# Performance work log

Measured on AMD Instinct MI355X. Metric: run time of the kernel, lower is better.

The kernel has to match this reference:

```python
import jax, jax.numpy as jnp
import numpy as np

NSUB = 2          # fixed RK4 substeps per output interval (deterministic stand-in for adaptive dopri5)
SLOPE = 1.0 / 5.5  # leaky_relu negative slope used by g and OutputNN


def setup_inputs() -> dict:
    key = jax.random.key(0)
    ks = iter(jax.random.split(key, 40))
    B, Tp, Tf = 256, 32, 256
    D, H, HF, HG, HO = 1, 100, 275, 75, 75

    def rn(shape, s=0.05):
        return jax.random.normal(next(ks), shape, jnp.float32) * s

    # past: [B, Tp, 1+D] with strictly increasing times in column 0
    past_t = jnp.sort(jax.random.uniform(next(ks), (B, Tp), jnp.float32) * Tp, axis=1)
    past_x = jax.random.normal(next(ks), (B, Tp, D), jnp.float32)
    past = jnp.concatenate([past_t[:, :, None], past_x], axis=2)
    # future times start after the last past time, strictly increasing
    t_future = past_t[:, -1:] + jnp.sort(
        jax.random.uniform(next(ks), (B, Tf), jnp.float32) * 0.1 * Tf, axis=1)

    return dict(
        past=past,
        h0=jnp.zeros((B, H), jnp.float32),
        t_future=t_future,
        eps=jax.random.normal(next(ks), (H, B), jnp.float32),
        fW1=rn((HF, H + 1)), fb1=rn((HF,)), fW2=rn((HF, HF)), fb2=rn((HF,)),
        fW3=rn((H, HF)), fb3=rn((H,)),
        gru_Wih=rn((3 * H, D)), gru_Whh=rn((3 * H, H)),
        gru_bih=rn((3 * H,)), gru_bhh=rn((3 * H,)),
        gW1=rn((HG, H)), gb1=rn((HG,)), gW2=rn((HG, HG)), gb2=rn((HG,)),
        gW3=rn((2, HG)), gb3=rn((2,)),
        oW1=rn((HO, H)), ob1=rn((HO,)), oW2=rn((HO, HO)), ob2=rn((HO,)),
        oW3=rn((D, HO)), ob3=rn((D,)),
    )


def _leaky(x):
    return jnp.where(x >= 0, x, SLOPE * x)


def reference(past, h0, t_future, eps,
              fW1, fb1, fW2, fb2, fW3, fb3,
              gru_Wih, gru_Whh, gru_bih, gru_bhh,
              gW1, gb1, gW2, gb2, gW3, gb3,
              oW1, ob1, oW2, ob2, oW3, ob3):
    def field(t, y):  # t: [B], y: [B, H] -> dy/dt: [B, H]  (f module)
        x = jnp.concatenate([t[:, None], y], axis=1)
        x = jnp.tanh(x @ fW1.T + fb1)
        x = jnp.tanh(x @ fW2.T + fb2)
        return jnp.tanh(x @ fW3.T + fb3)

    def integrate(y0, t0, t1):  # batched fixed-step RK4 from t0 to t1 (per-batch times)
        dt = ((t1 - t0) / NSUB)[:, None]  # [B, 1]
        dts = dt[:, 0]
        def body(y, i):
            t = t0 + i * dts
            k1 = field(t, y)
            k2 = field(t + 0.5 * dts, y + 0.5 * dt * k1)
            k3 = field(t + 0.5 * dts, y + 0.5 * dt * k2)
            k4 = field(t + dts, y + dt * k3)
            return y + dt * (k1 + 2.0 * k2 + 2.0 * k3 + k4) / 6.0, None
        y, _ = jax.lax.scan(body, y0, jnp.arange(NSUB, dtype=y0.dtype))
        return y

    def gru(x, h):  # torch.nn.GRUCell math
        gi = x @ gru_Wih.T + gru_bih
        gh = h @ gru_Whh.T + gru_bhh
        ir, iz, inn = jnp.split(gi, 3, axis=1)
        hr, hz, hn = jnp.split(gh, 3, axis=1)
        r = jax.nn.sigmoid(ir + hr)
        z = jax.nn.sigmoid(iz + hz)
        n = jnp.tanh(inn + r * hn)
        return (1.0 - z) * n + z * h

    times = past[:, :, 0]   # [B, Tp]
    data = past[:, :, 1:]   # [B, Tp, D]

    # first GRUODE step: evolve h0 from t0-1 to t0, then GRU update with x0
    h = gru(data[:, 0], integrate(h0, times[:, 0] - 1.0, times[:, 0]))
    xs = (jnp.swapaxes(data[:, 1:], 0, 1), times[:, :-1].T, times[:, 1:].T)
    def pbody(hc, s):
        x, tp, tc = s
        return gru(x, integrate(hc, tp, tc)), None
    h, _ = jax.lax.scan(pbody, h, xs)

    # g head -> (loc, |scale|), reproducing the concat/view of the original
    gx = _leaky(h @ gW1.T + gb1)
    gx = _leaky(gx @ gW2.T + gb2)
    gx = gx @ gW3.T + gb3                                   # [B, 2]
    pr = jnp.concatenate([gx[:, 0], jnp.abs(gx[:, 1])]).reshape(-1, 2)
    loc, scale = pr[:, 0], pr[:, 1]                          # [B], [B]

    # Sampler: Normal(loc, scale).rsample([H]) reparameterized with eps [H, B]
    z0 = (loc[None, :] + scale[None, :] * eps).T             # [B, H]

    # integrate z0 across future time grid
    def fbody(y, s):
        tp, tc = s
        yn = integrate(y, tp, tc)
        return yn, yn
    _, traj = jax.lax.scan(fbody, z0, (t_future[:, :-1].T, t_future[:, 1:].T))
    out = jnp.swapaxes(jnp.concatenate([z0[None], traj], axis=0), 0, 1)  # [B, Tf, H]

    # OutputNN head
    o = _leaky(out @ oW1.T + ob1)
    o = _leaky(o @ oW2.T + ob2)
    return o @ oW3.T + ob3  # [B, Tf, D]
```

## Files before the change

### kernel.cpp

```cpp
#include <hip/hip_runtime.h>
#include <hip/hip_fp16.h>

typedef _Float16 f16;
typedef _Float16 f16x2 __attribute__((ext_vector_type(2)));
typedef _Float16 f16x8 __attribute__((ext_vector_type(8)));
typedef float f32x4 __attribute__((ext_vector_type(4)));
typedef unsigned short u16;
typedef unsigned int u32;

__device__ __forceinline__ float fdot2v(f16x2 a, f16x2 b, float c){
#if __has_builtin(__builtin_amdgcn_fdot2)
  return __builtin_amdgcn_fdot2(a, b, c, false);
#else
  return c + (float)a.x * (float)b.x + (float)a.y * (float)b.y;
#endif
}

__device__ __forceinline__ float rcp_f(float x){
#if __has_builtin(__builtin_amdgcn_rcpf)
  return __builtin_amdgcn_rcpf(x);
#else
  return 1.f / x;
#endif
}

__device__ __forceinline__ float tanh_f(float x){
  return 1.f - 2.f * rcp_f(__expf(2.f * x) + 1.f);
}
__device__ __forceinline__ float sigm_f(float x){
  return rcp_f(1.f + __expf(-x));
}
__device__ __forceinline__ float leaky_f(float x){
  return x >= 0.f ? x : x * (1.0f / 5.5f);
}

template<int NP>
__device__ __forceinline__ void ld_pairs(const float* W, int row, int ncols, int c0,
                                         f16x2* dst, bool valid){
  const float* base = W + (long)row * ncols;
#pragma unroll
  for (int p = 0; p < NP; p++){
    int c = c0 + 2 * p;
    f16x2 v;
    v.x = (valid && c     < ncols) ? (f16)base[c]     : (f16)0.f;
    v.y = (valid && c + 1 < ncols) ? (f16)base[c + 1] : (f16)0.f;
    dst[p] = v;
  }
}

template<int NCH>
__device__ __forceinline__ float dot_chunks(const f16x2* w, const f16x8* x, int chunk0){
  float a0 = 0.f, a1 = 0.f, a2 = 0.f, a3 = 0.f;
#pragma unroll
  for (int c = 0; c < NCH; c++){
    union { f16x8 v; f16x2 h[4]; } u;
    u.v = x[chunk0 + c];
    a0 = fdot2v(w[4*c + 0], u.h[0], a0);
    a1 = fdot2v(w[4*c + 1], u.h[1], a1);
    a2 = fdot2v(w[4*c + 2], u.h[2], a2);
    a3 = fdot2v(w[4*c + 3], u.h[3], a3);
  }
  return (a0 + a1) + (a2 + a3);
}

__device__ __forceinline__ f16x8 ldfrag(const float* W, int row, int ncols, int k0, bool valid){
  f16x8 v;
#pragma unroll
  for (int j = 0; j < 8; j++){
    int c = k0 + j;
    v[j] = (valid && c < ncols) ? (f16)W[(long)row * ncols + c] : (f16)0.f;
  }
  return v;
}

__device__ __forceinline__ float sel4(f32x4 a, int c){
  float v = a.x;
  v = (c == 1) ? a.y : v;
  v = (c == 2) ? a.z : v;
  v = (c == 3) ? a.w : v;
  return v;
}
__device__ __forceinline__ float selacc(f32x4 a0, f32x4 a1, int lm){
  f32x4 t;
  t.x = (lm & 4) ? a1.x : a0.x;
  t.y = (lm & 4) ? a1.y : a0.y;
  t.z = (lm & 4) ? a1.z : a0.z;
  t.w = (lm & 4) ? a1.w : a0.w;
  return sel4(t, lm & 3);
}

#define MFMA16(A,B,C) __builtin_amdgcn_mfma_f32_16x16x32_f16((A),(B),(C),0,0,0)

struct FRM {
  f16x8 a1[2][4];
  f16x8 a2[2][9];
  f16x8 a3[9];
  f16x2 w1b[4];
  f16x2 w2b[9];
  float w1tb, b1bv, b2bv;
  float w1tw, b1w, b2w;
  float b3w;
};

struct DEC {
  f16x2 dW1[16]; f16x2 dW2[12]; f16x2 dW3;
  float ob1v, ob2v, ob3v;
};

__device__ __forceinline__ void load_field_mfma(FRM& R, int tid,
    const float* fW1, const float* fb1, const float* fW2, const float* fb2,
    const float* fW3, const float* fb3)
{
  const int lane = tid & 63, wv = tid >> 6;
  const int lm = lane & 15, lg = lane >> 4;
  const int r0 = 32 * wv + lm, r1 = r0 + 16;
#pragma unroll
  for (int c = 0; c < 4; c++){
    R.a1[0][c] = ldfrag(fW1, r0, 101, 32 * c + 8 * lg, true);
    R.a1[1][c] = ldfrag(fW1, r1, 101, 32 * c + 8 * lg, true);
  }
#pragma unroll
  for (int c = 0; c < 9; c++){
    R.a2[0][c] = ldfrag(fW2, r0, 275, 32 * c + 8 * lg, true);
    R.a2[1][c] = ldfrag(fW2, r1, 275, 32 * c + 8 * lg, true);
  }
  const int r3 = 16 * wv + lm;
  const bool v3 = (wv < 7) && (r3 < 100);
#pragma unroll
  for (int c = 0; c < 9; c++)
    R.a3[c] = ldfrag(fW3, v3 ? r3 : 0, 275, 32 * c + 8 * lg, v3);

  const bool p2 = tid < 304;
  const int m = tid >> 4, s = tid & 15;
  const int j2 = 256 + m;
  ld_pairs<4>(fW1, p2 ? j2 : 0, 101, 8 * s, R.w1b, p2);
  R.w1tb = (p2 && s == 0) ? fW1[j2 * 101] : 0.f;
  R.b1bv = p2 ? fb1[j2] : 0.f;
  ld_pairs<9>(fW2, p2 ? j2 : 0, 275, 18 * s, R.w2b, p2);
  R.b2bv = p2 ? fb2[j2] : 0.f;

  const int lmw = lm & 7;
  const int rwc = 32 * wv + 16 * (lmw >> 2) + 4 * lg + (lmw & 3);
  R.w1tw = fW1[rwc * 101];
  R.b1w  = fb1[rwc];
  R.b2w  = fb2[rwc];
  const int r3w = 16 * wv + 4 * lg + (lm & 3);
  R.b3w = ((wv < 7) && (r3w < 100)) ? fb3[r3w] : 0.f;
}

template<bool D>
__device__ __forceinline__ f32x4 field_eval_m(const FRM& R, const DEC& dc,
    float t, int tid, f16* ust, f16* x1s, f16* x2s,
    const f16x8* yv, f16* o1s, f16* o2s, float* outp, int tf)
{
  const int lm = tid & 15, lg = (tid >> 4) & 3, wv = tid >> 6;
  const f16x8* ub  = (const f16x8*)ust;
  const f16x8* x1b = (const f16x8*)x1s;
  const f16x8* x2b = (const f16x8*)x2s;
  const f32x4 zz = {0.f, 0.f, 0.f, 0.f};

  {
    f32x4 p0 = zz, p1 = zz, q0 = zz, q1 = zz;
#pragma unroll
    for (int c = 0; c < 2; c++){
      f16x8 bp = ub[4 * c + lg];
      f16x8 bq = ub[4 * (c + 2) + lg];
      p0 = MFMA16(R.a1[0][c],     bp, p0);
      p1 = MFMA16(R.a1[1][c],     bp, p1);
      q0 = MFMA16(R.a1[0][c + 2], bq, q0);
      q1 = MFMA16(R.a1[1][c + 2], bq, q1);
    }
    if (tid < 304){
      int s = tid & 15;
      float a2 = (s == 0) ? R.w1tb * t : 0.f;
      const f16x2* uv2 = (const f16x2*)ust + 4 * s;
#pragma unroll
      for (int p = 0; p < 4; p++) a2 = fdot2v(R.w1b[p], uv2[p], a2);
      a2 += __shfl_xor(a2, 1); a2 += __shfl_xor(a2, 2);
      a2 += __shfl_xor(a2, 4); a2 += __shfl_xor(a2, 8);
      if (s == 0) x1s[256 + (tid >> 4)] = (f16)tanh_f(a2 + R.b1bv);
    }
    if (D){
      int jq = tid >> 2, qq = tid & 3;
      if (jq < 75){
        float a = dot_chunks<4>(dc.dW1, yv, 4 * qq);
        a += __shfl_xor(a, 1); a += __shfl_xor(a, 2);
        if (qq == 0) o1s[jq] = (f16)leaky_f(a + dc.ob1v);
      }
    }
    f32x4 acc0 = p0 + q0, acc1 = p1 + q1;
    if (lm < 8){
      int rw = 32 * wv + 16 * (lm >> 2) + 4 * lg + (lm & 3);
      float v = selacc(acc0, acc1, lm);
      x1s[rw] = (f16)tanh_f(v + R.w1tw * t + R.b1w);
    }
  }
  __syncthreads();

  {
    f32x4 p0 = zz, p1 = zz, q0 = zz, q1 = zz;
#pragma unroll
    for (int c = 0; c < 4; c++){
      f16x8 bp = x1b[4 * c + lg];
      f16x8 bq = x1b[4 * (c + 5) + lg];
      p0 = MFMA16(R.a2[0][c],     bp, p0);
      p1 = MFMA16(R.a2[1][c],     bp, p1);
      q0 = MFMA16(R.a2[0][c + 5], bq, q0);
      q1 = MFMA16(R.a2[1][c + 5], bq, q1);
    }
    {
      f16x8 bp = x1b[16 + lg];
      p0 = MFMA16(R.a2[0][4], bp, p0);
      p1 = MFMA16(R.a2[1][4], bp, p1);
    }
    if (tid < 304){
      int s = tid & 15;
      float a2 = 0.f;
      const f16x2* xv2 = (const f16x2*)x1s + 9 * s;
#pragma unroll
      for (int p = 0; p < 9; p++) a2 = fdot2v(R.w2b[p], xv2[p], a2);
      a2 += __shfl_xor(a2, 1); a2 += __shfl_xor(a2, 2);
      a2 += __shfl_xor(a2, 4); a2 += __shfl_xor(a2, 8);
      if (s == 0) x2s[256 + (tid >> 4)] = (f16)tanh_f(a2 + R.b2bv);
    }
    if (D){
      int jq = tid >> 2, qq = tid & 3;
      if (jq < 75){
        float a = dot_chunks<3>(dc.dW2, (const f16x8*)o1s, 3 * qq);
        a += __shfl_xor(a, 1); a += __shfl_xor(a, 2);
        if (qq == 0) o2s[jq] = (f16)leaky_f(a + dc.ob2v);
      }
    }
    f32x4 acc0 = p0 + q0, acc1 = p1 + q1;
    if (lm < 8){
      int rw = 32 * wv + 16 * (lm >> 2) + 4 * lg + (lm & 3);
      float v = selacc(acc0, acc1, lm);
      x2s[rw] = (f16)tanh_f(v + R.b2w);
    }
  }
  __syncthreads();

  f32x4 acc3 = zz;
  if (wv < 7){
    f32x4 r0 = zz, r1 = zz;
#pragma unroll
    for (int c = 0; c < 4; c++){
      r0 = MFMA16(R.a3[c],     x2b[4 * c + lg], r0);
      r1 = MFMA16(R.a3[c + 5], x2b[4 * (c + 5) + lg], r1);
    }
    r0 = MFMA16(R.a3[4], x2b[16 + lg], r0);
    acc3 = r0 + r1;
  }
  if (D){
    if (tid >= 448){
      int t2 = tid - 448;
      float a = 0.f;
      if (t2 < 40) a = fdot2v(dc.dW3, ((const f16x2*)o2s)[t2], 0.f);
      a += __shfl_xor(a, 1);  a += __shfl_xor(a, 2);  a += __shfl_xor(a, 4);
      a += __shfl_xor(a, 8);  a += __shfl_xor(a, 16); a += __shfl_xor(a, 32);
      if (t2 == 0) outp[tf] = a + dc.ob3v;
    }
  }
  return acc3;
}

__global__ __launch_bounds__(512, 2) void k_encode(
    const float* __restrict__ past, const float* __restrict__ h0,
    const float* __restrict__ fW1, const float* __restrict__ fb1,
    const float* __restrict__ fW2, const float* __restrict__ fb2,
    const float* __restrict__ fW3, const float* __restrict__ fb3,
    const float* __restrict__ Wih, const float* __restrict__ Whh,
    const float* __restrict__ bih, const float* __restrict__ bhh,
    const float* __restrict__ gW1, const float* __restrict__ gb1,
    const float* __restrict__ gW2, const float* __restrict__ gb2,
    const float* __restrict__ gW3, const float* __restrict__ gb3,
    float* __restrict__ gx_ws)
{
  __shared__ f16x8 ustV[16];
  __shared__ f16x8 ystV[16];
  __shared__ f16x8 x1V[36];
  __shared__ f16x8 x2V[36];
  __shared__ float yf[100];
  __shared__ float ghs[300];
  __shared__ f16x2 gW1s[75 * 52];
  __shared__ f16x2 gW2s[75 * 40];
  __shared__ f16x2 gW3s[80];
  __shared__ f16x2 g1s2[40];
  __shared__ f16x2 g2s2[40];

  const int tid = threadIdx.x;
  const int b = blockIdx.x;
  f16* ust = (f16*)ustV;
  f16* yst = (f16*)ystV;
  f16* x1s = (f16*)x1V;
  f16* x2s = (f16*)x2V;
  f16* g1s = (f16*)g1s2;
  f16* g2s = (f16*)g2s2;

  FRM R;
  load_field_mfma(R, tid, fW1, fb1, fW2, fb2, fW3, fb3);
  DEC dcz{};

  f16x2 whh[28]; float bhhv;
  f16x2 whhb[7]; float bhhbv;
  {
    int j1 = tid >> 1, h = tid & 1;
    ld_pairs<28>(Whh, j1, 100, 56 * h, whh, true);
    bhhv = bhh[j1];
    bool p2 = tid < 352;
    int j2 = 256 + (tid >> 3), s7 = tid & 7;
    ld_pairs<7>(Whh, p2 ? j2 : 0, 100, 14 * s7, whhb, p2);
    bhhbv = p2 ? bhh[j2] : 0.f;
  }
  float wihr=0,wihz=0,wihn=0,bihr=0,bihz=0,bihn=0;
  if (tid < 100){
    wihr = Wih[tid];       bihr = bih[tid];
    wihz = Wih[tid + 100]; bihz = bih[tid + 100];
    wihn = Wih[tid + 200]; bihn = bih[tid + 200];
  }
  const int jq = tid >> 2, qq = tid & 3;
  const bool lv = (qq == 0 && jq < 75);
  float gb1v = lv ? gb1[jq] : 0.f;
  float gb2v = lv ? gb2[jq] : 0.f;

  for (int i = tid; i < 75 * 52; i += 512){
    int r = i / 52, c = 2 * (i % 52);
    f16x2 v;
    v.x = (c     < 100) ? (f16)gW1[r * 100 + c]     : (f16)0.f;
    v.y = (c + 1 < 100) ? (f16)gW1[r * 100 + c + 1] : (f16)0.f;
    gW1s[i] = v;
  }
  for (int i = tid; i < 75 * 40; i += 512){
    int r = i / 40, c = 2 * (i % 40);
    f16x2 v;
    v.x = (c     < 75) ? (f16)gW2[r * 75 + c]     : (f16)0.f;
    v.y = (c + 1 < 75) ? (f16)gW2[r * 75 + c + 1] : (f16)0.f;
    gW2s[i] = v;
  }
  for (int i = tid; i < 80; i += 512){
    int r = i / 40, c = 2 * (i % 40);
    f16x2 v;
    v.x = (c     < 75) ? (f16)gW3[r * 75 + c]     : (f16)0.f;
    v.y = (c + 1 < 75) ? (f16)gW3[r * 75 + c + 1] : (f16)0.f;
    gW3s[i] = v;
  }
  for (int i = tid; i < 128; i += 512){ ust[i] = (f16)0.f; yst[i] = (f16)0.f; }
  for (int i = tid; i < 288; i += 512){ x1s[i] = (f16)0.f; x2s[i] = (f16)0.f; }
  for (int i = tid; i < 80;  i += 512){ g1s[i] = (f16)0.f; g2s[i] = (f16)0.f; }
  if (tid < 100){
    float v = h0[b * 100 + tid];
    yf[tid] = v; yst[tid] = (f16)v; ust[1 + tid] = (f16)v;
  }
  __syncthreads();

  const int lm = tid & 15, lg2 = (tid >> 4) & 3, wv = tid >> 6;
  const int row3 = 16 * wv + 4 * lg2 + (lm & 3);
  const bool wr3 = (lm < 4) && (wv < 7) && (row3 < 100);
  float k1v = 0.f, k2v = 0.f, k3v = 0.f;

  auto rk_interval = [&](float tp, float tc){
    float dts = (tc - tp) * 0.5f;
#pragma unroll 1
    for (int sub = 0; sub < 2; sub++){
      float t0 = tp + sub * dts;
      float yfr = 0.f;
      __syncthreads();
      if (wr3) yfr = yf[row3];
      f32x4 a = field_eval_m<false>(R, dcz, t0, tid, ust, x1s, x2s,
                                    nullptr, nullptr, nullptr, nullptr, 0);
      if (wr3){ float kv = tanh_f(sel4(a, lm) + R.b3w); k1v = kv;
                ust[1 + row3] = (f16)(yfr + 0.5f * dts * kv); }
      __syncthreads();
      a = field_eval_m<false>(R, dcz, t0 + 0.5f * dts, tid, ust, x1s, x2s,
                              nullptr, nullptr, nullptr, nullptr, 0);
      if (wr3){ float kv = tanh_f(sel4(a, lm) + R.b3w); k2v = kv;
                ust[1 + row3] = (f16)(yfr + 0.5f * dts * kv); }
      __syncthreads();
      a = field_eval_m<false>(R, dcz, t0 + 0.5f * dts, tid, ust, x1s, x2s,
                              nullptr, nullptr, nullptr, nullptr, 0);
      if (wr3){ float kv = tanh_f(sel4(a, lm) + R.b3w); k3v = kv;
                ust[1 + row3] = (f16)(yfr + dts * kv); }
      __syncthreads();
      a = field_eval_m<false>(R, dcz, t0 + dts, tid, ust, x1s, x2s,
                              nullptr, nullptr, nullptr, nullptr, 0);
      if (wr3){
        float kv = tanh_f(sel4(a, lm) + R.b3w);
        float yn = yfr + dts * (k1v + 2.f * (k2v + k3v) + kv) * (1.f / 6.f);
        yf[row3] = yn; ust[1 + row3] = (f16)yn; yst[row3] = (f16)yn;
      }
    }
  };

  const float* prow = past + b * 64;
#pragma unroll 1
  for (int st = 0; st < 32; st++){
    float tc = prow[2 * st];
    float tp = (st == 0) ? (tc - 1.f) : prow[2 * st - 2];
    rk_interval(tp, tc);
    __syncthreads();
    {
      int j1 = tid >> 1, h = tid & 1;
      float a = dot_chunks<7>(whh, ystV, 7 * h);
      a += __shfl_xor(a, 1);
      if (!h) ghs[j1] = a + bhhv;
      if (tid < 352){
        int s7 = tid & 7;
        float a2 = 0.f;
        const f16x2* yv2 = (const f16x2*)ystV + 7 * s7;
#pragma unroll
        for (int p = 0; p < 7; p++) a2 = fdot2v(whhb[p], yv2[p], a2);
        a2 += __shfl_xor(a2, 1); a2 += __shfl_xor(a2, 2); a2 += __shfl_xor(a2, 4);
        if (s7 == 0) ghs[256 + (tid >> 3)] = a2 + bhhbv;
      }
    }
    __syncthreads();
    if (tid < 100){
      float x = prow[2 * st + 1];
      float r = sigm_f(x * wihr + bihr + ghs[tid]);
      float z = sigm_f(x * wihz + bihz + ghs[tid + 100]);
      float n = tanh_f(x * wihn + bihn + r * ghs[tid + 200]);
      float hn = (1.f - z) * n + z * yf[tid];
      yf[tid] = hn; yst[tid] = (f16)hn; ust[1 + tid] = (f16)hn;
    }
  }

  __syncthreads();
  {
    float a = 0.f;
    const f16x2* yv = (const f16x2*)ystV + 13 * qq;
    if (jq < 75){
#pragma unroll
      for (int p = 0; p < 13; p++) a = fdot2v(gW1s[jq * 52 + 13 * qq + p], yv[p], a);
    }
    a += __shfl_xor(a, 1); a += __shfl_xor(a, 2);
    if (lv) g1s[jq] = (f16)leaky_f(a + gb1v);
  }
  __syncthreads();
  {
    float a = 0.f;
    const f16x2* xv = (const f16x2*)g1s + 10 * qq;
    if (jq < 75){
#pragma unroll
      for (int p = 0; p < 10; p++) a = fdot2v(gW2s[jq * 40 + 10 * qq + p], xv[p], a);
    }
    a += __shfl_xor(a, 1); a += __shfl_xor(a, 2);
    if (lv) g2s[jq] = (f16)leaky_f(a + gb2v);
  }
  __syncthreads();
  if (tid < 2){
    const f16x2* g2v = (const f16x2*)g2s;
    float a = gb3[tid];
    for (int p = 0; p < 40; p++) a = fdot2v(gW3s[tid * 40 + p], g2v[p], a);
    gx_ws[b * 2 + tid] = a;
  }
}

__global__ __launch_bounds__(512, 2) void k_forecast(
    const float* __restrict__ t_future, const float* __restrict__ eps,
    const float* __restrict__ fW1, const float* __restrict__ fb1,
    const float* __restrict__ fW2, const float* __restrict__ fb2,
    const float* __restrict__ fW3, const float* __restrict__ fb3,
    const float* __restrict__ oW1, const float* __restrict__ ob1,
    const float* __restrict__ oW2, const float* __restrict__ ob2,
    const float* __restrict__ oW3, const float* __restrict__ ob3,
    const float* __restrict__ gx_ws, float* __restrict__ out)
{
  __shared__ f16x8 ustV[16];
  __shared__ f16x8 ystV[16];
  __shared__ f16x8 x1V[36];
  __shared__ f16x8 x2V[36];
  __shared__ f16x8 o1V[12];
  __shared__ f16x8 o2V[12];

  const int tid = threadIdx.x;
  const int b = blockIdx.x;
  f16* ust = (f16*)ustV;
  f16* yst = (f16*)ystV;
  f16* x1s = (f16*)x1V;
  f16* x2s = (f16*)x2V;
  f16* o1s = (f16*)o1V;
  f16* o2s = (f16*)o2V;
  float* outb = out + b * 256;

  FRM R;
  load_field_mfma(R, tid, fW1, fb1, fW2, fb2, fW3, fb3);

  const int jq = tid >> 2, qq = tid & 3;
  const bool dv = jq < 75;
  const bool lv = (qq == 0 && dv);
  DEC dc;
  ld_pairs<16>(oW1, dv ? jq : 0, 100, 32 * qq, dc.dW1, dv);
  ld_pairs<12>(oW2, dv ? jq : 0, 75, 24 * qq, dc.dW2, dv);
  {
    int t2 = tid - 448;
    bool v = (t2 >= 0 && t2 < 40);
    ld_pairs<1>(oW3, 0, 75, v ? 2 * t2 : 0, &dc.dW3, v);
  }
  dc.ob1v = lv ? ob1[jq] : 0.f;
  dc.ob2v = lv ? ob2[jq] : 0.f;
  dc.ob3v = ob3[0];

  for (int i = tid; i < 128; i += 512){ ust[i] = (f16)0.f; yst[i] = (f16)0.f; }
  for (int i = tid; i < 288; i += 512){ x1s[i] = (f16)0.f; x2s[i] = (f16)0.f; }
  for (int i = tid; i < 96;  i += 512){ o1s[i] = (f16)0.f; o2s[i] = (f16)0.f; }

  const int lm = tid & 15, lg2 = (tid >> 4) & 3, wv = tid >> 6;
  const int row3 = 16 * wv + 4 * lg2 + (lm & 3);
  const bool wr3 = (lm < 4) && (wv < 7) && (row3 < 100);
  float k1v = 0.f, k2v = 0.f, k3v = 0.f, yfr = 0.f;

  if (wr3){
    float loc, scl;
    if (b < 128){ loc = gx_ws[4 * b];              scl = gx_ws[4 * b + 2]; }
    else        { loc = fabsf(gx_ws[4 * b - 511]); scl = fabsf(gx_ws[4 * b - 509]); }
    float e = eps[row3 * 256 + b];
    yfr = loc + scl * e;
    yst[row3] = (f16)yfr; ust[1 + row3] = (f16)yfr;
  }
  __syncthreads();

  const float* trow = t_future + b * 256;
#pragma unroll 1
  for (int iv = 0; iv < 255; iv++){
    float tp = trow[iv];
    float tc = trow[iv + 1];
    float dts = (tc - tp) * 0.5f;
#pragma unroll 1
    for (int sub = 0; sub < 2; sub++){
      float t0 = tp + sub * dts;
      __syncthreads();
      f32x4 a;
      if (sub == 0)
        a = field_eval_m<true >(R, dc, t0, tid, ust, x1s, x2s,
                                (const f16x8*)yst, o1s, o2s, outb, iv);
      else
        a = field_eval_m<false>(R, dc, t0, tid, ust, x1s, x2s,
                                nullptr, nullptr, nullptr, nullptr, 0);
      if (wr3){ float kv = tanh_f(sel4(a, lm) + R.b3w); k1v = kv;
                ust[1 + row3] = (f16)(yfr + 0.5f * dts * kv); }
      __syncthreads();
      a = field_eval_m<false>(R, dc, t0 + 0.5f * dts, tid, ust, x1s, x2s,
                              nullptr, nullptr, nullptr, nullptr, 0);
      if (wr3){ float kv = tanh_f(sel4(a, lm) + R.b3w); k2v = kv;
                ust[1 + row3] = (f16)(yfr + 0.5f * dts * kv); }
      __syncthreads();
      a = field_eval_m<false>(R, dc, t0 + 0.5f * dts, tid, ust, x1s, x2s,
                              nullptr, nullptr, nullptr, nullptr, 0);
      if (wr3){ float kv = tanh_f(sel4(a, lm) + R.b3w); k3v = kv;
                ust[1 + row3] = (f16)(yfr + dts * kv); }
      __syncthreads();
      a = field_eval_m<false>(R, dc, t0 + dts, tid, ust, x1s, x2s,
                              nullptr, nullptr, nullptr, nullptr, 0);
      if (wr3){
        float kv = tanh_f(sel4(a, lm) + R.b3w);
        float yn = yfr + dts * (k1v + 2.f * (k2v + k3v) + kv) * (1.f / 6.f);
        yfr = yn; ust[1 + row3] = (f16)yn; yst[row3] = (f16)yn;
      }
    }
  }

  __syncthreads();
  if (dv){
    float a = dot_chunks<4>(dc.dW1, (const f16x8*)yst, 4 * qq);
    a += __shfl_xor(a, 1); a += __shfl_xor(a, 2);
    if (qq == 0) o1s[jq] = (f16)leaky_f(a + dc.ob1v);
  }
  __syncthreads();
  if (dv){
    float a = dot_chunks<3>(dc.dW2, (const f16x8*)o1s, 3 * qq);
    a += __shfl_xor(a, 1); a += __shfl_xor(a, 2);
    if (qq == 0) o2s[jq] = (f16)leaky_f(a + dc.ob2v);
  }
  __syncthreads();
  if (tid >= 448){
    int t2 = tid - 448;
    float a = 0.f;
    if (t2 < 40) a = fdot2v(dc.dW3, ((const f16x2*)o2s)[t2], 0.f);
    a += __shfl_xor(a, 1);  a += __shfl_xor(a, 2);  a += __shfl_xor(a, 4);
    a += __shfl_xor(a, 8);  a += __shfl_xor(a, 16); a += __shfl_xor(a, 32);
    if (t2 == 0) outb[255] = a + dc.ob3v;
  }
}

extern "C" void kernel_launch(void* const* d_in, const int* in_sizes, int n_in,
                              void* d_out, int out_size, void* d_ws, size_t ws_size,
                              hipStream_t stream) {
  (void)in_sizes; (void)n_in; (void)out_size; (void)ws_size;
  const float* past     = (const float*)d_in[0];
  const float* h0       = (const float*)d_in[1];
  const float* t_future = (const float*)d_in[2];
  const float* eps      = (const float*)d_in[3];
  const float* fW1 = (const float*)d_in[4];  const float* fb1 = (const float*)d_in[5];
  const float* fW2 = (const float*)d_in[6];  const float* fb2 = (const float*)d_in[7];
  const float* fW3 = (const float*)d_in[8];  const float* fb3 = (const float*)d_in[9];
  const float* Wih = (const float*)d_in[10]; const float* Whh = (const float*)d_in[11];
  const float* bih = (const float*)d_in[12]; const float* bhh = (const float*)d_in[13];
  const float* gW1 = (const float*)d_in[14]; const float* gb1 = (const float*)d_in[15];
  const float* gW2 = (const float*)d_in[16]; const float* gb2 = (const float*)d_in[17];
  const float* gW3 = (const float*)d_in[18]; const float* gb3 = (const float*)d_in[19];
  const float* oW1 = (const float*)d_in[20]; const float* ob1 = (const float*)d_in[21];
  const float* oW2 = (const float*)d_in[22]; const float* ob2 = (const float*)d_in[23];
  const float* oW3 = (const float*)d_in[24]; const float* ob3 = (const float*)d_in[25];
  float* gxws = (float*)d_ws;
  float* out = (float*)d_out;

  hipLaunchKernelGGL(k_encode, dim3(256), dim3(512), 0, stream,
      past, h0, fW1, fb1, fW2, fb2, fW3, fb3,
      Wih, Whh, bih, bhh, gW1, gb1, gW2, gb2, gW3, gb3, gxws);
  hipLaunchKernelGGL(k_forecast, dim3(256), dim3(512), 0, stream,
      t_future, eps, fW1, fb1, fW2, fb2, fW3, fb3,
      oW1, ob1, oW2, ob2, oW3, ob3, gxws, out);
}
```

Measured before the change: 3.894 ms.

## Rebalance field MLP work: MFMA tail rows in waves 6-7, scalar last rows of layer 3

Rows 256-274 of layers 1 and 2 were computed with scalar fdot2 and shuffle reductions on 304 threads. They now go through an extra MFMA tile in waves 6 and 7, using a register array that reuses the layer-3 fragment slot. Layer 3 is now done by MFMA in waves 0-5 only, while wave 7 computes rows 96-99 with fdot2 and shuffles, and the decoder's final dot product moves to wave 6. This is meant to shorten the critical path of each field evaluation and remove the scalar reduction overhead, at the cost of uneven register use and more per-wave branching.

```diff
diff --git a/kernel.cpp b/kernel.cpp
--- a/kernel.cpp
+++ b/kernel.cpp
@@ -80,24 +80,14 @@
   v = (c == 3) ? a.w : v;
   return v;
 }
-__device__ __forceinline__ float selacc(f32x4 a0, f32x4 a1, int lm){
-  f32x4 t;
-  t.x = (lm & 4) ? a1.x : a0.x;
-  t.y = (lm & 4) ? a1.y : a0.y;
-  t.z = (lm & 4) ? a1.z : a0.z;
-  t.w = (lm & 4) ? a1.w : a0.w;
-  return sel4(t, lm & 3);
-}
 
 #define MFMA16(A,B,C) __builtin_amdgcn_mfma_f32_16x16x32_f16((A),(B),(C),0,0,0)
 
 struct FRM {
   f16x8 a1[2][4];
   f16x8 a2[2][9];
-  f16x8 a3[9];
-  f16x2 w1b[4];
-  f16x2 w2b[9];
-  float w1tb, b1bv, b2bv;
+  f16x8 af[13];
+  f16x2 w3b[9];
   float w1tw, b1w, b2w;
   float b3w;
 };
@@ -124,28 +114,41 @@
     R.a2[0][c] = ldfrag(fW2, r0, 275, 32 * c + 8 * lg, true);
     R.a2[1][c] = ldfrag(fW2, r1, 275, 32 * c + 8 * lg, true);
   }
-  const int r3 = 16 * wv + lm;
-  const bool v3 = (wv < 7) && (r3 < 100);
-#pragma unroll
-  for (int c = 0; c < 9; c++)
-    R.a3[c] = ldfrag(fW3, v3 ? r3 : 0, 275, 32 * c + 8 * lg, v3);
-
-  const bool p2 = tid < 304;
-  const int m = tid >> 4, s = tid & 15;
-  const int j2 = 256 + m;
-  ld_pairs<4>(fW1, p2 ? j2 : 0, 101, 8 * s, R.w1b, p2);
-  R.w1tb = (p2 && s == 0) ? fW1[j2 * 101] : 0.f;
-  R.b1bv = p2 ? fb1[j2] : 0.f;
-  ld_pairs<9>(fW2, p2 ? j2 : 0, 275, 18 * s, R.w2b, p2);
-  R.b2bv = p2 ? fb2[j2] : 0.f;
-
-  const int lmw = lm & 7;
-  const int rwc = 32 * wv + 16 * (lmw >> 2) + 4 * lg + (lmw & 3);
-  R.w1tw = fW1[rwc * 101];
-  R.b1w  = fb1[rwc];
-  R.b2w  = fb2[rwc];
-  const int r3w = 16 * wv + 4 * lg + (lm & 3);
-  R.b3w = ((wv < 7) && (r3w < 100)) ? fb3[r3w] : 0.f;
+  if (wv < 6){
+    const int r3 = 16 * wv + lm;
+#pragma unroll
+    for (int c = 0; c < 9; c++)
+      R.af[c] = ldfrag(fW3, r3, 275, 32 * c + 8 * lg, true);
+#pragma unroll
+    for (int c = 9; c < 13; c++) R.af[c] = (f16x8)(f16)0.f;
+  } else {
+    const int r2 = 256 + 16 * (wv - 6) + lm;
+    const bool v2 = r2 < 275;
+    const int r2c = v2 ? r2 : 0;
+#pragma unroll
+    for (int c = 0; c < 4; c++)
+      R.af[c] = ldfrag(fW1, r2c, 101, 32 * c + 8 * lg, v2);
+#pragma unroll
+    for (int c = 0; c < 9; c++)
+      R.af[4 + c] = ldfrag(fW2, r2c, 275, 32 * c + 8 * lg, v2);
+  }
+  {
+    const bool w7 = (wv == 7);
+    ld_pairs<9>(fW3, w7 ? (96 + lg) : 0, 275, 18 * lm, R.w3b, w7);
+  }
+  {
+    const int s = lm >> 2;
+    const bool use3 = (s == 2) && (wv >= 6);
+    int rw = use3 ? (256 + 16 * (wv - 6) + 4 * lg + (lm & 3))
+                  : (32 * wv + 16 * (s & 1) + 4 * lg + (lm & 3));
+    int rwc = rw < 275 ? rw : 274;
+    R.w1tw = fW1[rwc * 101];
+    R.b1w  = fb1[rwc];
+    R.b2w  = fb2[rwc];
+  }
+  if (wv < 6)       R.b3w = fb3[16 * wv + 4 * lg + (lm & 3)];
+  else if (wv == 7) R.b3w = fb3[96 + lg];
+  else              R.b3w = 0.f;
 }
 
 template<bool D>
@@ -154,31 +157,23 @@
     const f16x8* yv, f16* o1s, f16* o2s, float* outp, int tf)
 {
   const int lm = tid & 15, lg = (tid >> 4) & 3, wv = tid >> 6;
+  const bool x3 = (wv >= 6);
+  const int nw = x3 ? 12 : 8;
   const f16x8* ub  = (const f16x8*)ust;
   const f16x8* x1b = (const f16x8*)x1s;
   const f16x8* x2b = (const f16x8*)x2s;
   const f32x4 zz = {0.f, 0.f, 0.f, 0.f};
 
   {
-    f32x4 p0 = zz, p1 = zz, q0 = zz, q1 = zz;
-#pragma unroll
-    for (int c = 0; c < 2; c++){
-      f16x8 bp = ub[4 * c + lg];
-      f16x8 bq = ub[4 * (c + 2) + lg];
-      p0 = MFMA16(R.a1[0][c],     bp, p0);
-      p1 = MFMA16(R.a1[1][c],     bp, p1);
-      q0 = MFMA16(R.a1[0][c + 2], bq, q0);
-      q1 = MFMA16(R.a1[1][c + 2], bq, q1);
-    }
-    if (tid < 304){
-      int s = tid & 15;
-      float a2 = (s == 0) ? R.w1tb * t : 0.f;
-      const f16x2* uv2 = (const f16x2*)ust + 4 * s;
-#pragma unroll
-      for (int p = 0; p < 4; p++) a2 = fdot2v(R.w1b[p], uv2[p], a2);
-      a2 += __shfl_xor(a2, 1); a2 += __shfl_xor(a2, 2);
-      a2 += __shfl_xor(a2, 4); a2 += __shfl_xor(a2, 8);
-      if (s == 0) x1s[256 + (tid >> 4)] = (f16)tanh_f(a2 + R.b1bv);
+    f16x8 u0 = ub[lg], u1 = ub[4 + lg], u2 = ub[8 + lg], u3 = ub[12 + lg];
+    f32x4 A0 = zz, A1 = zz, A2 = zz, B0 = zz, B1 = zz, B2 = zz;
+    A0 = MFMA16(R.a1[0][0], u0, A0);  A1 = MFMA16(R.a1[1][0], u0, A1);
+    B0 = MFMA16(R.a1[0][1], u1, B0);  B1 = MFMA16(R.a1[1][1], u1, B1);
+    A0 = MFMA16(R.a1[0][2], u2, A0);  A1 = MFMA16(R.a1[1][2], u2, A1);
+    B0 = MFMA16(R.a1[0][3], u3, B0);  B1 = MFMA16(R.a1[1][3], u3, B1);
+    if (x3){
+      A2 = MFMA16(R.af[0], u0, A2);  B2 = MFMA16(R.af[1], u1, B2);
+      A2 = MFMA16(R.af[2], u2, A2);  B2 = MFMA16(R.af[3], u3, B2);
     }
     if (D){
       int jq = tid >> 2, qq = tid & 3;
@@ -188,40 +183,32 @@
         if (qq == 0) o1s[jq] = (f16)leaky_f(a + dc.ob1v);
       }
     }
-    f32x4 acc0 = p0 + q0, acc1 = p1 + q1;
-    if (lm < 8){
-      int rw = 32 * wv + 16 * (lm >> 2) + 4 * lg + (lm & 3);
-      float v = selacc(acc0, acc1, lm);
+    if (lm < nw){
+      int s = lm >> 2, reg = lm & 3;
+      int rw = (s == 2) ? (256 + 16 * (wv - 6) + 4 * lg + reg)
+                        : (32 * wv + 16 * s + 4 * lg + reg);
+      float v0 = sel4(A0 + B0, reg), v1 = sel4(A1 + B1, reg), v2 = sel4(A2 + B2, reg);
+      float v = (s == 0) ? v0 : ((s == 1) ? v1 : v2);
       x1s[rw] = (f16)tanh_f(v + R.w1tw * t + R.b1w);
     }
   }
   __syncthreads();
 
   {
-    f32x4 p0 = zz, p1 = zz, q0 = zz, q1 = zz;
-#pragma unroll
-    for (int c = 0; c < 4; c++){
+    f32x4 A0 = zz, A1 = zz, A2 = zz, B0 = zz, B1 = zz, B2 = zz;
+#pragma unroll
+    for (int c = 0; c < 5; c++){
       f16x8 bp = x1b[4 * c + lg];
-      f16x8 bq = x1b[4 * (c + 5) + lg];
-      p0 = MFMA16(R.a2[0][c],     bp, p0);
-      p1 = MFMA16(R.a2[1][c],     bp, p1);
-      q0 = MFMA16(R.a2[0][c + 5], bq, q0);
-      q1 = MFMA16(R.a2[1][c + 5], bq, q1);
-    }
-    {
-      f16x8 bp = x1b[16 + lg];
-      p0 = MFMA16(R.a2[0][4], bp, p0);
-      p1 = MFMA16(R.a2[1][4], bp, p1);
-    }
-    if (tid < 304){
-      int s = tid & 15;
-      float a2 = 0.f;
-      const f16x2* xv2 = (const f16x2*)x1s + 9 * s;
-#pragma unroll
-      for (int p = 0; p < 9; p++) a2 = fdot2v(R.w2b[p], xv2[p], a2);
-      a2 += __shfl_xor(a2, 1); a2 += __shfl_xor(a2, 2);
-      a2 += __shfl_xor(a2, 4); a2 += __shfl_xor(a2, 8);
-      if (s == 0) x2s[256 + (tid >> 4)] = (f16)tanh_f(a2 + R.b2bv);
+      A0 = MFMA16(R.a2[0][c], bp, A0);
+      A1 = MFMA16(R.a2[1][c], bp, A1);
+      if (x3) A2 = MFMA16(R.af[4 + c], bp, A2);
+    }
+#pragma unroll
+    for (int c = 5; c < 9; c++){
+      f16x8 bq = x1b[4 * c + lg];
+      B0 = MFMA16(R.a2[0][c], bq, B0);
+      B1 = MFMA16(R.a2[1][c], bq, B1);
+      if (x3) B2 = MFMA16(R.af[4 + c], bq, B2);
     }
     if (D){
       int jq = tid >> 2, qq = tid & 3;
@@ -231,29 +218,37 @@
         if (qq == 0) o2s[jq] = (f16)leaky_f(a + dc.ob2v);
       }
     }
-    f32x4 acc0 = p0 + q0, acc1 = p1 + q1;
-    if (lm < 8){
-      int rw = 32 * wv + 16 * (lm >> 2) + 4 * lg + (lm & 3);
-      float v = selacc(acc0, acc1, lm);
+    if (lm < nw){
+      int s = lm >> 2, reg = lm & 3;
+      int rw = (s == 2) ? (256 + 16 * (wv - 6) + 4 * lg + reg)
+                        : (32 * wv + 16 * s + 4 * lg + reg);
+      float v0 = sel4(A0 + B0, reg), v1 = sel4(A1 + B1, reg), v2 = sel4(A2 + B2, reg);
+      float v = (s == 0) ? v0 : ((s == 1) ? v1 : v2);
       x2s[rw] = (f16)tanh_f(v + R.b2w);
     }
   }
   __syncthreads();
 
   f32x4 acc3 = zz;
-  if (wv < 7){
+  if (wv < 6){
     f32x4 r0 = zz, r1 = zz;
 #pragma unroll
-    for (int c = 0; c < 4; c++){
-      r0 = MFMA16(R.a3[c],     x2b[4 * c + lg], r0);
-      r1 = MFMA16(R.a3[c + 5], x2b[4 * (c + 5) + lg], r1);
-    }
-    r0 = MFMA16(R.a3[4], x2b[16 + lg], r0);
+    for (int c = 0; c < 5; c++) r0 = MFMA16(R.af[c], x2b[4 * c + lg], r0);
+#pragma unroll
+    for (int c = 5; c < 9; c++) r1 = MFMA16(R.af[c], x2b[4 * c + lg], r1);
     acc3 = r0 + r1;
+  } else if (wv == 7){
+    float a2t = 0.f;
+    const f16x2* xv2 = (const f16x2*)x2s + 9 * lm;
+#pragma unroll
+    for (int p = 0; p < 9; p++) a2t = fdot2v(R.w3b[p], xv2[p], a2t);
+    a2t += __shfl_xor(a2t, 1); a2t += __shfl_xor(a2t, 2);
+    a2t += __shfl_xor(a2t, 4); a2t += __shfl_xor(a2t, 8);
+    acc3.x = a2t;
   }
   if (D){
-    if (tid >= 448){
-      int t2 = tid - 448;
+    if (wv == 6){
+      int t2 = tid - 384;
       float a = 0.f;
       if (t2 < 40) a = fdot2v(dc.dW3, ((const f16x2*)o2s)[t2], 0.f);
       a += __shfl_xor(a, 1);  a += __shfl_xor(a, 2);  a += __shfl_xor(a, 4);
@@ -354,9 +349,16 @@
   __syncthreads();
 
   const int lm = tid & 15, lg2 = (tid >> 4) & 3, wv = tid >> 6;
-  const int row3 = 16 * wv + 4 * lg2 + (lm & 3);
-  const bool wr3 = (lm < 4) && (wv < 7) && (row3 < 100);
+  bool wr3; int row3;
+  if (wv < 6)      { wr3 = (lm < 4);  row3 = 16 * wv + 4 * lg2 + (lm & 3); }
+  else if (wv == 7){ wr3 = (lm == 0); row3 = 96 + lg2; }
+  else             { wr3 = false;     row3 = 0; }
   float k1v = 0.f, k2v = 0.f, k3v = 0.f;
+
+  auto kval = [&](f32x4 a){
+    float av = (wv == 7) ? a.x : sel4(a, lm);
+    return tanh_f(av + R.b3w);
+  };
 
   auto rk_interval = [&](float tp, float tc){
     float dts = (tc - tp) * 0.5f;
@@ -368,23 +370,23 @@
       if (wr3) yfr = yf[row3];
       f32x4 a = field_eval_m<false>(R, dcz, t0, tid, ust, x1s, x2s,
                                     nullptr, nullptr, nullptr, nullptr, 0);
-      if (wr3){ float kv = tanh_f(sel4(a, lm) + R.b3w); k1v = kv;
+      if (wr3){ float kv = kval(a); k1v = kv;
                 ust[1 + row3] = (f16)(yfr + 0.5f * dts * kv); }
       __syncthreads();
       a = field_eval_m<false>(R, dcz, t0 + 0.5f * dts, tid, ust, x1s, x2s,
                               nullptr, nullptr, nullptr, nullptr, 0);
-      if (wr3){ float kv = tanh_f(sel4(a, lm) + R.b3w); k2v = kv;
+      if (wr3){ float kv = kval(a); k2v = kv;
                 ust[1 + row3] = (f16)(yfr + 0.5f * dts * kv); }
       __syncthreads();
       a = field_eval_m<false>(R, dcz, t0 + 0.5f * dts, tid, ust, x1s, x2s,
                               nullptr, nullptr, nullptr, nullptr, 0);
-      if (wr3){ float kv = tanh_f(sel4(a, lm) + R.b3w); k3v = kv;
+      if (wr3){ float kv = kval(a); k3v = kv;
                 ust[1 + row3] = (f16)(yfr + dts * kv); }
       __syncthreads();
       a = field_eval_m<false>(R, dcz, t0 + dts, tid, ust, x1s, x2s,
                               nullptr, nullptr, nullptr, nullptr, 0);
       if (wr3){
-        float kv = tanh_f(sel4(a, lm) + R.b3w);
+        float kv = kval(a);
         float yn = yfr + dts * (k1v + 2.f * (k2v + k3v) + kv) * (1.f / 6.f);
         yf[row3] = yn; ust[1 + row3] = (f16)yn; yst[row3] = (f16)yn;
       }
@@ -492,7 +494,7 @@
   ld_pairs<16>(oW1, dv ? jq : 0, 100, 32 * qq, dc.dW1, dv);
   ld_pairs<12>(oW2, dv ? jq : 0, 75, 24 * qq, dc.dW2, dv);
   {
-    int t2 = tid - 448;
+    int t2 = tid - 384;
     bool v = (t2 >= 0 && t2 < 40);
     ld_pairs<1>(oW3, 0, 75, v ? 2 * t2 : 0, &dc.dW3, v);
   }
@@ -505,9 +507,16 @@
   for (int i = tid; i < 96;  i += 512){ o1s[i] = (f16)0.f; o2s[i] = (f16)0.f; }
 
   const int lm = tid & 15, lg2 = (tid >> 4) & 3, wv = tid >> 6;
-  const int row3 = 16 * wv + 4 * lg2 + (lm & 3);
-  const bool wr3 = (lm < 4) && (wv < 7) && (row3 < 100);
+  bool wr3; int row3;
+  if (wv < 6)      { wr3 = (lm < 4);  row3 = 16 * wv + 4 * lg2 + (lm & 3); }
+  else if (wv == 7){ wr3 = (lm == 0); row3 = 96 + lg2; }
+  else             { wr3 = false;     row3 = 0; }
   float k1v = 0.f, k2v = 0.f, k3v = 0.f, yfr = 0.f;
+
+  auto kval = [&](f32x4 a){
+    float av = (wv == 7) ? a.x : sel4(a, lm);
+    return tanh_f(av + R.b3w);
+  };
 
   if (wr3){
     float loc, scl;
@@ -536,23 +545,23 @@
       else
         a = field_eval_m<false>(R, dc, t0, tid, ust, x1s, x2s,
                                 nullptr, nullptr, nullptr, nullptr, 0);
-      if (wr3){ float kv = tanh_f(sel4(a, lm) + R.b3w); k1v = kv;
+      if (wr3){ float kv = kval(a); k1v = kv;
                 ust[1 + row3] = (f16)(yfr + 0.5f * dts * kv); }
       __syncthreads();
       a = field_eval_m<false>(R, dc, t0 + 0.5f * dts, tid, ust, x1s, x2s,
                               nullptr, nullptr, nullptr, nullptr, 0);
-      if (wr3){ float kv = tanh_f(sel4(a, lm) + R.b3w); k2v = kv;
+      if (wr3){ float kv = kval(a); k2v = kv;
                 ust[1 + row3] = (f16)(yfr + 0.5f * dts * kv); }
       __syncthreads();
       a = field_eval_m<false>(R, dc, t0 + 0.5f * dts, tid, ust, x1s, x2s,
                               nullptr, nullptr, nullptr, nullptr, 0);
-      if (wr3){ float kv = tanh_f(sel4(a, lm) + R.b3w); k3v = kv;
+      if (wr3){ float kv = kval(a); k3v = kv;
                 ust[1 + row3] = (f16)(yfr + dts * kv); }
       __syncthreads();
       a = field_eval_m<false>(R, dc, t0 + dts, tid, ust, x1s, x2s,
                               nullptr, nullptr, nullptr, nullptr, 0);
       if (wr3){
-        float kv = tanh_f(sel4(a, lm) + R.b3w);
+        float kv = kval(a);
         float yn = yfr + dts * (k1v + 2.f * (k2v + k3v) + kv) * (1.f / 6.f);
         yfr = yn; ust[1 + row3] = (f16)yn; yst[row3] = (f16)yn;
       }
@@ -572,8 +581,8 @@
     if (qq == 0) o2s[jq] = (f16)leaky_f(a + dc.ob2v);
   }
   __syncthreads();
-  if (tid >= 448){
-    int t2 = tid - 448;
+  if (wv == 6){
+    int t2 = tid - 384;
     float a = 0.f;
     if (t2 < 40) a = fdot2v(dc.dW3, ((const f16x2*)o2s)[t2], 0.f);
     a += __shfl_xor(a, 1);  a += __shfl_xor(a, 2);  a += __shfl_xor(a, 4);
```

Result: faster. 3.489 ms (-10.4%).
